# Performance work log

Hardware: AMD Instinct MI355X
Metric: run time of the kernel (lower is better)

## Reference

```python
import jax, jax.numpy as jnp
import numpy as np

N, K, DIN, DOUT = 50000, 16, 128, 64  # nodes per graph, fixed in-degree, feature dims


def setup_inputs() -> dict:
    key = jax.random.key(0)
    ks = jax.random.split(key, 9)
    s1 = 1.0 / np.sqrt(DIN)
    s2 = 1.0 / np.sqrt(2 * DOUT)
    return {
        "x1": jax.random.normal(ks[0], (N, DIN), jnp.float32),
        "x2": jax.random.normal(ks[1], (N, DIN), jnp.float32),
        "nbr1": jax.random.randint(ks[2], (N, K), 0, N, dtype=jnp.int32),
        "nbr2": jax.random.randint(ks[3], (N, K), 0, N, dtype=jnp.int32),
        "W_e1": jax.random.uniform(ks[4], (DIN, DOUT), jnp.float32, -s1, s1),
        "W_s1": jax.random.uniform(ks[5], (DIN, DOUT), jnp.float32, -s1, s1),
        "W_e2": jax.random.uniform(ks[6], (2 * DOUT, DOUT), jnp.float32, -s2, s2),
        "W_s2": jax.random.uniform(ks[7], (2 * DOUT, DOUT), jnp.float32, -s2, s2),
        "w_att": jax.random.uniform(ks[8], (2 * DOUT,), jnp.float32, -s2, s2),
    }


def _layer(x, nbr, We, Ws, norm):
    # CGNNConv: per-edge-type linear on sources, self linear on dests,
    # norm-weighted scatter-add aggregation, sigmoid(cat(self, aggr)).
    xn = x @ We                                      # [N, DOUT] source transform
    xs = x @ Ws                                      # [N, DOUT] self transform
    aggr = jnp.sum(norm[..., None] * xn[nbr], axis=1)  # [N, DOUT] fixed-degree segment sum
    return jax.nn.sigmoid(jnp.concatenate([xs, aggr], axis=1)), aggr


def _self_attn(aggr, nbr, w):
    # exp(leaky_relu(cat(aggr[dst], aggr[src]) @ w)), normalized over each dst's in-edges
    si = aggr @ w[:DOUT]            # dest contribution, [N]
    sj = (aggr @ w[DOUT:])[nbr]     # src contribution,  [N, K]
    e = jnp.exp(jax.nn.leaky_relu(si[:, None] + sj, 0.01))
    return e / jnp.sum(e, axis=1, keepdims=True)


def _cross_attn(aggr1, nbr1, aggr2, nbr2):
    # pairwise exp(-||a1_k - a2_l||) over each paired node's neighbor sets,
    # normalized by the total sum; att1 = row marginals, att2 = col marginals.
    a1, a2 = aggr1[nbr1], aggr2[nbr2]                # [N, K, DOUT]
    d2 = (jnp.sum(a1 * a1, -1)[:, :, None] + jnp.sum(a2 * a2, -1)[:, None, :]
          - 2.0 * jnp.einsum('nkd,nld->nkl', a1, a2))
    sim = jnp.exp(-jnp.sqrt(jnp.maximum(d2, 1e-12)))  # [N, K, K]
    total = jnp.sum(sim, axis=(1, 2), keepdims=True)  # [N, 1, 1]
    att1 = jnp.sum(sim, axis=2) / total[:, :, 0]      # [N, K]
    att2 = jnp.sum(sim, axis=1) / total[:, 0, :]      # [N, K]
    return att1, att2


def reference(x1, x2, nbr1, nbr2, W_e1, W_s1, W_e2, W_s2, w_att):
    inv_deg = jnp.full((N, K), 1.0 / K, dtype=x1.dtype)  # degree(col)^-1 with fixed degree K
    # layers 0 .. num_layers-2 use degree norm (shared weights across both graphs)
    h1, aggr1 = _layer(x1, nbr1, W_e1, W_s1, inv_deg)
    h2, aggr2 = _layer(x2, nbr2, W_e1, W_s1, inv_deg)
    # attention stages on last aggregates
    sa1 = _self_attn(aggr1, nbr1, w_att)
    sa2 = _self_attn(aggr2, nbr2, w_att)
    ca1, ca2 = _cross_attn(aggr1, nbr1, aggr2, nbr2)
    # final layer uses norm = cross_attention * self_attention per edge
    o1, _ = _layer(h1, nbr1, W_e2, W_s2, ca1 * sa1)
    o2, _ = _layer(h2, nbr2, W_e2, W_s2, ca2 * sa2)
    return o1, o2
```

## Files before the change

### kernel.cpp

```cpp
#include <hip/hip_runtime.h>
#include <hip/hip_bf16.h>

#define N_NODES 50000
#define K_NBR   16
#define DIN     128
#define DOUT    64
#define NPB     64

typedef __hip_bfloat16 bf16;
typedef __attribute__((ext_vector_type(8))) short bf16x8;
typedef __attribute__((ext_vector_type(4))) float f32x4;

__device__ __forceinline__ float b2f(bf16 v) { return __bfloat162float(v); }
__device__ __forceinline__ float us2f(unsigned short u) {
    return __uint_as_float(((unsigned)u) << 16);
}
__device__ __forceinline__ float sigmoidf_(float x) { return 1.0f / (1.0f + __expf(-x)); }
__device__ __forceinline__ short f2bs(float f) {
    bf16 b = __float2bfloat16(f);
    return *reinterpret_cast<short*>(&b);
}
__device__ __forceinline__ float readlane_f(float v, int lane) {
    return __uint_as_float(__builtin_amdgcn_readlane(__float_as_uint(v), lane));
}

template <typename T> __device__ __forceinline__ float ld(const T* p, size_t i);
template <> __device__ __forceinline__ float ld<float>(const float* p, size_t i) { return p[i]; }
template <> __device__ __forceinline__ float ld<bf16>(const bf16* p, size_t i)   { return b2f(p[i]); }

template <typename T> __device__ __forceinline__ void st(T* p, size_t i, float v);
template <> __device__ __forceinline__ void st<float>(float* p, size_t i, float v) { p[i] = v; }
template <> __device__ __forceinline__ void st<bf16>(bf16* p, size_t i, float v)   { p[i] = __float2bfloat16(v); }

__device__ __forceinline__ bf16x8 load_a8(const bf16* p) { return *(const bf16x8*)p; }
__device__ __forceinline__ bf16x8 load_a8(const float* p) {
    float4 v0 = *(const float4*)p;
    float4 v1 = *(const float4*)(p + 4);
    bf16x8 r;
    r[0] = f2bs(v0.x); r[1] = f2bs(v0.y); r[2] = f2bs(v0.z); r[3] = f2bs(v0.w);
    r[4] = f2bs(v1.x); r[5] = f2bs(v1.y); r[6] = f2bs(v1.z); r[7] = f2bs(v1.w);
    return r;
}

__global__ __launch_bounds__(256) void wtrans_kernel(
    const void* __restrict__ Wa, const void* __restrict__ Wb,
    const void* __restrict__ Wc, const void* __restrict__ Wd,
    const unsigned short* __restrict__ x1probe,
    unsigned short* __restrict__ wtg, int* __restrict__ flag)
{
    __shared__ unsigned short t[DIN][DOUT + 1];
    __shared__ int cnt;
    if (threadIdx.x == 0) cnt = 0;
    __syncthreads();
    int c = 0;
#pragma unroll
    for (int i = 0; i < 16; ++i) {
        unsigned short w = x1probe[(size_t)(threadIdx.x * 16 + i) * 2];
        int e = (w >> 7) & 0xFF;
        c += (e >= 112 && e <= 142) ? 1 : 0;
    }
    atomicAdd(&cnt, c);
    __syncthreads();
    const int isf32 = (cnt >= 2048) ? 0 : 1;
    if (blockIdx.x == 0 && threadIdx.x == 0) *flag = isf32;

    const void* W = (blockIdx.x == 0 ? Wa : blockIdx.x == 1 ? Wb : blockIdx.x == 2 ? Wc : Wd);
    unsigned short* o = wtg + (size_t)blockIdx.x * DIN * DOUT;
    if (isf32) {
        const float* Wf = (const float*)W;
#pragma unroll 8
        for (int it = 0; it < 32; ++it) {
            int idx = threadIdx.x + 256 * it;
            t[idx >> 6][idx & 63] = (unsigned short)f2bs(Wf[idx]);
        }
    } else {
        const unsigned short* Wh = (const unsigned short*)W;
#pragma unroll 8
        for (int it = 0; it < 32; ++it) {
            int idx = threadIdx.x + 256 * it;
            t[idx >> 6][idx & 63] = Wh[idx];
        }
    }
    __syncthreads();
#pragma unroll 8
    for (int it = 0; it < 32; ++it) {
        int idx = threadIdx.x + 256 * it;
        int d = idx >> 7, k = idx & 127;
        o[idx] = t[k][d];
    }
}

template <typename TX, typename TO>
__device__ __forceinline__ void lin_mfma_body(
    const TX* __restrict__ x,
    const unsigned short* __restrict__ wt2,
    bf16* __restrict__ xnh, TO* __restrict__ o,
    unsigned short* __restrict__ wt)
{
    const int tid = threadIdx.x;
    const int nbase = blockIdx.x * NPB;

#pragma unroll
    for (int it = 0; it < 8; ++it) {
        int idx = tid + 256 * it;
        int mt = idx >> 10, rem = idx & 1023;
        int r = rem >> 4, c = rem & 15;
        int4 v = *(const int4*)(wt2 + mt * 8192 + r * DIN + c * 8);
        *(int4*)(wt + mt * 8192 + r * DIN + ((c ^ (r & 15)) << 3)) = v;
    }
    __syncthreads();

    const int w = tid >> 6, lane = tid & 63;
    const int m = lane & 15, g = lane >> 4;

    int arow = nbase + w * 16 + m;
    if (arow >= N_NODES) arow = N_NODES - 1;
    const TX* xrow = x + (size_t)arow * DIN;

    f32x4 acc[2][4] = {};
#pragma unroll
    for (int ks = 0; ks < 4; ++ks) {
        bf16x8 a = load_a8(xrow + ks * 32 + g * 8);
        int slot = ((ks * 4 + g) ^ m) << 3;
#pragma unroll
        for (int mt = 0; mt < 2; ++mt)
#pragma unroll
        for (int nc = 0; nc < 4; ++nc) {
            bf16x8 b = *(const bf16x8*)(wt + mt * 8192 + (nc * 16 + m) * DIN + slot);
            acc[mt][nc] = __builtin_amdgcn_mfma_f32_16x16x32_bf16(a, b, acc[mt][nc], 0, 0, 0);
        }
    }

#pragma unroll
    for (int nc = 0; nc < 4; ++nc) {
#pragma unroll
        for (int j = 0; j < 4; ++j) {
            int n = nbase + w * 16 + g * 4 + j;
            if (n < N_NODES) {
                int d = nc * 16 + m;
                xnh[(size_t)n * DOUT + d] = __float2bfloat16(acc[0][nc][j]);
                st(o, (size_t)n * DIN + d, sigmoidf_(acc[1][nc][j]));
            }
        }
    }
}

__global__ __launch_bounds__(256) void lin1_kernel(
    const void* __restrict__ x1, const void* __restrict__ x2,
    const unsigned short* __restrict__ wtg,
    bf16* __restrict__ xnh1, bf16* __restrict__ xnh2,
    bf16* __restrict__ h1, bf16* __restrict__ h2,
    const int* __restrict__ flag)
{
    __shared__ __align__(16) unsigned short wt[2 * DOUT * DIN];
    const int g = blockIdx.y;
    const void* x   = g ? x2 : x1;
    bf16*       xnh = g ? xnh2 : xnh1;
    bf16*       h   = g ? h2 : h1;
    if (*flag) lin_mfma_body<float, bf16>((const float*)x, wtg, xnh, h, wt);
    else       lin_mfma_body<bf16,  bf16>((const bf16*)x,  wtg, xnh, h, wt);
}

__global__ __launch_bounds__(256) void lin2_kernel(
    const bf16* __restrict__ h1, const bf16* __restrict__ h2,
    const unsigned short* __restrict__ wtg,
    bf16* __restrict__ heh1, bf16* __restrict__ heh2,
    void* __restrict__ out, const int* __restrict__ flag)
{
    __shared__ __align__(16) unsigned short wt[2 * DOUT * DIN];
    const int g = blockIdx.y;
    const bf16* h   = g ? h2 : h1;
    bf16*       heh = g ? heh2 : heh1;
    if (*flag) lin_mfma_body<bf16, float>(h, wtg + 2 * 8192, heh,
                                          (float*)out + (size_t)g * N_NODES * DIN, wt);
    else       lin_mfma_body<bf16, bf16>(h, wtg + 2 * 8192, heh,
                                         (bf16*)out + (size_t)g * N_NODES * DIN, wt);
}

template <typename T>
__device__ __forceinline__ void aggr1_body(
    const int* __restrict__ nbr, const bf16* __restrict__ xnh,
    bf16* __restrict__ agh, bf16* __restrict__ h, const T* __restrict__ watt,
    float* __restrict__ qq, float* __restrict__ slo, float* __restrict__ shi)
{
    const int warp = __builtin_amdgcn_readfirstlane(threadIdx.x >> 6);
    const int lane = threadIdx.x & 63;
    const int n = blockIdx.x * 4 + warp;
    const int* __restrict__ nrow = nbr + n * K_NBR;
    const unsigned short* __restrict__ xu = (const unsigned short*)xnh;

    unsigned short xv[K_NBR];
#pragma unroll
    for (int k = 0; k < K_NBR; ++k)
        xv[k] = xu[(size_t)nrow[k] * DOUT + lane];

    float acc = 0.f;
#pragma unroll
    for (int k = 0; k < K_NBR; ++k) acc += us2f(xv[k]);
    acc *= (1.0f / K_NBR);
    bf16 av16 = __float2bfloat16(acc);
    float av = b2f(av16);
    agh[(size_t)n * DOUT + lane] = av16;
    h[(size_t)n * DIN + DOUT + lane] = __float2bfloat16(sigmoidf_(acc));

    float wl = ld(watt, lane);
    float wh = ld(watt, DOUT + lane);
    float pq = av * av;
    float pl = acc * wl;
    float ph = acc * wh;
#pragma unroll
    for (int off = 1; off < 64; off <<= 1) {
        pq += __shfl_xor(pq, off, 64);
        pl += __shfl_xor(pl, off, 64);
        ph += __shfl_xor(ph, off, 64);
    }
    if (lane == 0) { qq[n] = pq; slo[n] = pl; shi[n] = ph; }
}

__global__ __launch_bounds__(256) void aggr1_kernel(
    const int* __restrict__ nbr1, const int* __restrict__ nbr2,
    const bf16* __restrict__ xnh1, const bf16* __restrict__ xnh2,
    bf16* __restrict__ agh1, bf16* __restrict__ agh2,
    bf16* __restrict__ h1, bf16* __restrict__ h2,
    const void* __restrict__ watt,
    float* __restrict__ qq1, float* __restrict__ qq2,
    float* __restrict__ slo1, float* __restrict__ slo2,
    float* __restrict__ shi1, float* __restrict__ shi2,
    const int* __restrict__ flag)
{
    const int g = blockIdx.y;
    const int*  nbr = g ? nbr2 : nbr1;
    const bf16* xnh = g ? xnh2 : xnh1;
    bf16*       agh = g ? agh2 : agh1;
    bf16*       h   = g ? h2 : h1;
    float* qq  = g ? qq2  : qq1;
    float* slo = g ? slo2 : slo1;
    float* shi = g ? shi2 : shi1;
    if (*flag) aggr1_body<float>(nbr, xnh, agh, h, (const float*)watt, qq, slo, shi);
    else       aggr1_body<bf16>(nbr, xnh, agh, h, (const bf16*)watt,  qq, slo, shi);
}

template <typename TO>
__device__ __forceinline__ void attn_fused_body(
    const int* __restrict__ nbr1, const int* __restrict__ nbr2,
    const unsigned short* __restrict__ agh1, const unsigned short* __restrict__ agh2,
    const float* __restrict__ qq1, const float* __restrict__ qq2,
    const float* __restrict__ slo1, const float* __restrict__ slo2,
    const float* __restrict__ shi1, const float* __restrict__ shi2,
    const bf16* __restrict__ heh1, const bf16* __restrict__ heh2,
    TO* __restrict__ out)
{
    const int warp = __builtin_amdgcn_readfirstlane(threadIdx.x >> 6);
    const int lane = threadIdx.x & 63;
    const int n = blockIdx.x * 4 + warp;
    const int m = lane & 15, g = lane >> 4;

    const int* __restrict__ nrow1 = nbr1 + n * K_NBR;
    const int* __restrict__ nrow2 = nbr2 + n * K_NBR;
    const unsigned short* __restrict__ hu1 = (const unsigned short*)heh1;
    const unsigned short* __restrict__ hu2 = (const unsigned short*)heh2;

    unsigned short hv1[K_NBR], hv2[K_NBR];
#pragma unroll
    for (int k = 0; k < K_NBR; ++k) {
        hv1[k] = hu1[(size_t)nrow1[k] * DOUT + lane];
        hv2[k] = hu2[(size_t)nrow2[k] * DOUT + lane];
    }

    int idxr = 0;
    if (lane < 32) idxr = ((lane < 16) ? nbr1 : nbr2)[n * K_NBR + m];

    const int i1 = __shfl(idxr, m, 64);
    const int i2 = __shfl(idxr, 16 + m, 64);

    const bf16x8* a1p = (const bf16x8*)(agh1 + (size_t)i1 * DOUT + g * 8);
    const bf16x8* a2p = (const bf16x8*)(agh2 + (size_t)i2 * DOUT + g * 8);
    bf16x8 aA = a1p[0], aB = a1p[4];
    bf16x8 bA = a2p[0], bB = a2p[4];

    int myidx = __shfl(idxr, lane & 31, 64);
    const float* pa = (lane < 16) ? qq1 : (lane < 32) ? qq2 : (lane < 48) ? shi1 : shi2;
    float aux = pa[(size_t)myidx];

    float si  = (lane < 16) ? slo1[n] : slo2[n];
    float sjv = __shfl(aux, 32 + (lane & 31), 64);
    float v = si + sjv;
    v = v > 0.f ? v : 0.01f * v;
    float ev = __expf(v);
    float esum = ev;
#pragma unroll
    for (int off = 1; off < 16; off <<= 1) esum += __shfl_xor(esum, off, 64);

    f32x4 acc = {};
    acc = __builtin_amdgcn_mfma_f32_16x16x32_bf16(aA, bA, acc, 0, 0, 0);
    acc = __builtin_amdgcn_mfma_f32_16x16x32_bf16(aB, bB, acc, 0, 0, 0);

    float q2c = __shfl(aux, 16 + m, 64);
    float s0, s1, s2, s3;
    {
        float q10 = __shfl(aux, g * 4 + 0, 64);
        float q11 = __shfl(aux, g * 4 + 1, 64);
        float q12 = __shfl(aux, g * 4 + 2, 64);
        float q13 = __shfl(aux, g * 4 + 3, 64);
        s0 = __expf(-sqrtf(fmaxf(q10 + q2c - 2.f * acc[0], 1e-12f)));
        s1 = __expf(-sqrtf(fmaxf(q11 + q2c - 2.f * acc[1], 1e-12f)));
        s2 = __expf(-sqrtf(fmaxf(q12 + q2c - 2.f * acc[2], 1e-12f)));
        s3 = __expf(-sqrtf(fmaxf(q13 + q2c - 2.f * acc[3], 1e-12f)));
    }

    float c = s0 + s1 + s2 + s3;
#pragma unroll
    for (int off = 1; off < 16; off <<= 1) {
        s0 += __shfl_xor(s0, off, 64);
        s1 += __shfl_xor(s1, off, 64);
        s2 += __shfl_xor(s2, off, 64);
        s3 += __shfl_xor(s3, off, 64);
    }
    float cs = c;
    cs += __shfl_xor(cs, 16, 64);
    cs += __shfl_xor(cs, 32, 64);
    float tot = cs;
#pragma unroll
    for (int off = 1; off < 16; off <<= 1) tot += __shfl_xor(tot, off, 64);
    float rt = 1.0f / tot;

    float r0 = __shfl(s0, (m >> 2) << 4, 64);
    float r1 = __shfl(s1, (m >> 2) << 4, 64);
    float r2 = __shfl(s2, (m >> 2) << 4, 64);
    float r3 = __shfl(s3, (m >> 2) << 4, 64);
    int mr = m & 3;
    float rsm = mr == 0 ? r0 : mr == 1 ? r1 : mr == 2 ? r2 : r3;

    float wv = (g == 0) ? (rsm * rt * ev / esum)
             : (g == 1) ? (cs  * rt * ev / esum) : 0.f;

    float acc1 = 0.f, acc2 = 0.f;
#pragma unroll
    for (int k = 0; k < K_NBR; ++k) {
        acc1 += readlane_f(wv, k)      * us2f(hv1[k]);
        acc2 += readlane_f(wv, 16 + k) * us2f(hv2[k]);
    }
    st(out, (size_t)n * DIN + DOUT + lane, sigmoidf_(acc1));
    st(out, ((size_t)N_NODES + n) * DIN + DOUT + lane, sigmoidf_(acc2));
}

__global__ __launch_bounds__(256) void attn_kernel(
    const int* __restrict__ nbr1, const int* __restrict__ nbr2,
    const unsigned short* __restrict__ agh1, const unsigned short* __restrict__ agh2,
    const float* __restrict__ qq1, const float* __restrict__ qq2,
    const float* __restrict__ slo1, const float* __restrict__ slo2,
    const float* __restrict__ shi1, const float* __restrict__ shi2,
    const bf16* __restrict__ heh1, const bf16* __restrict__ heh2,
    void* __restrict__ out, const int* __restrict__ flag)
{
    if (*flag) attn_fused_body<float>(nbr1, nbr2, agh1, agh2, qq1, qq2, slo1, slo2,
                                      shi1, shi2, heh1, heh2, (float*)out);
    else       attn_fused_body<bf16>(nbr1, nbr2, agh1, agh2, qq1, qq2, slo1, slo2,
                                     shi1, shi2, heh1, heh2, (bf16*)out);
}

extern "C" void kernel_launch(void* const* d_in, const int* in_sizes, int n_in,
                              void* d_out, int out_size, void* d_ws, size_t ws_size,
                              hipStream_t stream)
{
    const void* x1   = d_in[0];
    const void* x2   = d_in[1];
    const int*  nbr1 = (const int*)d_in[2];
    const int*  nbr2 = (const int*)d_in[3];
    const void* We1  = d_in[4];
    const void* Ws1  = d_in[5];
    const void* We2  = d_in[6];
    const void* Ws2  = d_in[7];
    const void* watt = d_in[8];

    char* ws = (char*)d_ws;
    const size_t SZH  = (size_t)N_NODES * DOUT * sizeof(bf16);
    const size_t HSZ  = (size_t)N_NODES * DIN * sizeof(bf16);
    const size_t NSZ  = (size_t)N_NODES * sizeof(float);
    bf16* xnh1 = (bf16*)(ws + 0 * SZH);
    bf16* xnh2 = (bf16*)(ws + 1 * SZH);
    bf16* agh1 = (bf16*)(ws + 2 * SZH);
    bf16* agh2 = (bf16*)(ws + 3 * SZH);
    bf16* h1   = (bf16*)(ws + 4 * SZH);
    bf16* h2   = (bf16*)(ws + 4 * SZH + HSZ);
    char* p    =         ws + 4 * SZH + 2 * HSZ;
    int*  flag = (int*)  (p);
    char* aux  =          p + 4096;
    float* qq1  = (float*)(aux + 0 * NSZ);
    float* qq2  = (float*)(aux + 1 * NSZ);
    float* slo1 = (float*)(aux + 2 * NSZ);
    float* slo2 = (float*)(aux + 3 * NSZ);
    float* shi1 = (float*)(aux + 4 * NSZ);
    float* shi2 = (float*)(aux + 5 * NSZ);
    unsigned short* wtg = (unsigned short*)(aux + 6 * NSZ);

    dim3 b(256);
    dim3 g4(N_NODES / 4, 2);
    dim3 gl((N_NODES + NPB - 1) / NPB, 2);
    dim3 ga(N_NODES / 4);

    wtrans_kernel<<<dim3(4), b, 0, stream>>>(We1, Ws1, We2, Ws2,
                                             (const unsigned short*)x1, wtg, flag);
    lin1_kernel <<<gl, b, 0, stream>>>(x1, x2, wtg, xnh1, xnh2, h1, h2, flag);
    aggr1_kernel<<<g4, b, 0, stream>>>(nbr1, nbr2, xnh1, xnh2, agh1, agh2, h1, h2,
                                       watt, qq1, qq2, slo1, slo2, shi1, shi2, flag);
    lin2_kernel <<<gl, b, 0, stream>>>(h1, h2, wtg, xnh1, xnh2, d_out, flag);
    attn_kernel <<<ga, b, 0, stream>>>(nbr1, nbr2, (const unsigned short*)agh1,
                                       (const unsigned short*)agh2, qq1, qq2,
                                       slo1, slo2, shi1, shi2, xnh1, xnh2,
                                       d_out, flag);
}
```

Measured before the change: 230.2 us.

## Fuse first-layer aggregation with second-layer MFMA linear into one kernel

Measured after the change: 251.3 us. +9.1%, slower.

```diff
diff --git a/kernel.cpp b/kernel.cpp
--- a/kernel.cpp
+++ b/kernel.cpp
@@ -94,7 +94,7 @@
 __device__ __forceinline__ void lin_mfma_body(
     const TX* __restrict__ x,
     const unsigned short* __restrict__ wt2,
-    bf16* __restrict__ xnh, TO* __restrict__ o,
+    bf16* __restrict__ xnh, TO* __restrict__ o, const int ostride,
     unsigned short* __restrict__ wt)
 {
     const int tid = threadIdx.x;
@@ -139,7 +139,7 @@
             if (n < N_NODES) {
                 int d = nc * 16 + m;
                 xnh[(size_t)n * DOUT + d] = __float2bfloat16(acc[0][nc][j]);
-                st(o, (size_t)n * DIN + d, sigmoidf_(acc[1][nc][j]));
+                st(o, (size_t)n * ostride + d, sigmoidf_(acc[1][nc][j]));
             }
         }
     }
@@ -149,95 +149,140 @@
     const void* __restrict__ x1, const void* __restrict__ x2,
     const unsigned short* __restrict__ wtg,
     bf16* __restrict__ xnh1, bf16* __restrict__ xnh2,
-    bf16* __restrict__ h1, bf16* __restrict__ h2,
+    bf16* __restrict__ hlo1, bf16* __restrict__ hlo2,
     const int* __restrict__ flag)
 {
     __shared__ __align__(16) unsigned short wt[2 * DOUT * DIN];
     const int g = blockIdx.y;
     const void* x   = g ? x2 : x1;
     bf16*       xnh = g ? xnh2 : xnh1;
-    bf16*       h   = g ? h2 : h1;
-    if (*flag) lin_mfma_body<float, bf16>((const float*)x, wtg, xnh, h, wt);
-    else       lin_mfma_body<bf16,  bf16>((const bf16*)x,  wtg, xnh, h, wt);
-}
-
-__global__ __launch_bounds__(256) void lin2_kernel(
-    const bf16* __restrict__ h1, const bf16* __restrict__ h2,
-    const unsigned short* __restrict__ wtg,
-    bf16* __restrict__ heh1, bf16* __restrict__ heh2,
-    void* __restrict__ out, const int* __restrict__ flag)
-{
-    __shared__ __align__(16) unsigned short wt[2 * DOUT * DIN];
-    const int g = blockIdx.y;
-    const bf16* h   = g ? h2 : h1;
-    bf16*       heh = g ? heh2 : heh1;
-    if (*flag) lin_mfma_body<bf16, float>(h, wtg + 2 * 8192, heh,
-                                          (float*)out + (size_t)g * N_NODES * DIN, wt);
-    else       lin_mfma_body<bf16, bf16>(h, wtg + 2 * 8192, heh,
-                                         (bf16*)out + (size_t)g * N_NODES * DIN, wt);
-}
-
-template <typename T>
-__device__ __forceinline__ void aggr1_body(
+    bf16*       hlo = g ? hlo2 : hlo1;
+    if (*flag) lin_mfma_body<float, bf16>((const float*)x, wtg, xnh, hlo, DOUT, wt);
+    else       lin_mfma_body<bf16,  bf16>((const bf16*)x,  wtg, xnh, hlo, DOUT, wt);
+}
+
+template <typename TW, typename TO>
+__device__ __forceinline__ void aggmm_body(
     const int* __restrict__ nbr, const bf16* __restrict__ xnh,
-    bf16* __restrict__ agh, bf16* __restrict__ h, const T* __restrict__ watt,
-    float* __restrict__ qq, float* __restrict__ slo, float* __restrict__ shi)
-{
-    const int warp = __builtin_amdgcn_readfirstlane(threadIdx.x >> 6);
-    const int lane = threadIdx.x & 63;
-    const int n = blockIdx.x * 4 + warp;
-    const int* __restrict__ nrow = nbr + n * K_NBR;
-    const unsigned short* __restrict__ xu = (const unsigned short*)xnh;
-
-    unsigned short xv[K_NBR];
-#pragma unroll
-    for (int k = 0; k < K_NBR; ++k)
-        xv[k] = xu[(size_t)nrow[k] * DOUT + lane];
-
-    float acc = 0.f;
-#pragma unroll
-    for (int k = 0; k < K_NBR; ++k) acc += us2f(xv[k]);
-    acc *= (1.0f / K_NBR);
-    bf16 av16 = __float2bfloat16(acc);
-    float av = b2f(av16);
-    agh[(size_t)n * DOUT + lane] = av16;
-    h[(size_t)n * DIN + DOUT + lane] = __float2bfloat16(sigmoidf_(acc));
+    const bf16* __restrict__ hlo, const unsigned short* __restrict__ wt2,
+    const TW* __restrict__ watt,
+    bf16* __restrict__ agh, float* __restrict__ qq, float* __restrict__ slo,
+    float* __restrict__ shi, bf16* __restrict__ heh, TO* __restrict__ out,
+    unsigned short* __restrict__ ht, unsigned short* __restrict__ wt)
+{
+    const int tid = threadIdx.x;
+    const int w = tid >> 6, lane = tid & 63;
+    const int nbase = blockIdx.x * NPB;
+
+#pragma unroll
+    for (int it = 0; it < 8; ++it) {
+        int idx = tid + 256 * it;
+        int mt = idx >> 10, rem = idx & 1023;
+        int r = rem >> 4, c = rem & 15;
+        int4 v = *(const int4*)(wt2 + mt * 8192 + r * DIN + c * 8);
+        *(int4*)(wt + mt * 8192 + r * DIN + ((c ^ (r & 15)) << 3)) = v;
+    }
 
     float wl = ld(watt, lane);
     float wh = ld(watt, DOUT + lane);
-    float pq = av * av;
-    float pl = acc * wl;
-    float ph = acc * wh;
-#pragma unroll
-    for (int off = 1; off < 64; off <<= 1) {
-        pq += __shfl_xor(pq, off, 64);
-        pl += __shfl_xor(pl, off, 64);
-        ph += __shfl_xor(ph, off, 64);
-    }
-    if (lane == 0) { qq[n] = pq; slo[n] = pl; shi[n] = ph; }
-}
-
-__global__ __launch_bounds__(256) void aggr1_kernel(
+    const unsigned short* __restrict__ xu = (const unsigned short*)xnh;
+    const unsigned short* __restrict__ hu = (const unsigned short*)hlo;
+
+#pragma unroll 4
+    for (int j = 0; j < 16; ++j) {
+        int n = nbase + w * 16 + j;
+        int ncl = n < N_NODES ? n : N_NODES - 1;
+        const int* __restrict__ nrow = nbr + ncl * K_NBR;
+        unsigned short xv[K_NBR];
+#pragma unroll
+        for (int k = 0; k < K_NBR; ++k)
+            xv[k] = xu[(size_t)nrow[k] * DOUT + lane];
+        unsigned short hl = hu[(size_t)ncl * DOUT + lane];
+
+        float acc = 0.f;
+#pragma unroll
+        for (int k = 0; k < K_NBR; ++k) acc += us2f(xv[k]);
+        acc *= (1.0f / K_NBR);
+        bf16 av16 = __float2bfloat16(acc);
+        float av = b2f(av16);
+
+        const int r = w * 16 + j;
+        ht[r * DIN + ((((lane >> 3) ^ j) << 3) | (lane & 7))] = hl;
+        ht[r * DIN + (((((lane >> 3) | 8) ^ j) << 3) | (lane & 7))] =
+            (unsigned short)f2bs(sigmoidf_(acc));
+
+        if (n < N_NODES) agh[(size_t)n * DOUT + lane] = av16;
+
+        float pq = av * av, pl = acc * wl, ph = acc * wh;
+#pragma unroll
+        for (int off = 1; off < 64; off <<= 1) {
+            pq += __shfl_xor(pq, off, 64);
+            pl += __shfl_xor(pl, off, 64);
+            ph += __shfl_xor(ph, off, 64);
+        }
+        if (lane == 0 && n < N_NODES) { qq[n] = pq; slo[n] = pl; shi[n] = ph; }
+    }
+    __syncthreads();
+
+    const int m = lane & 15, g = lane >> 4;
+    f32x4 acc2[2][4] = {};
+    const unsigned short* hrow = ht + (w * 16 + m) * DIN;
+#pragma unroll
+    for (int ks = 0; ks < 4; ++ks) {
+        int slot = ((ks * 4 + g) ^ m) << 3;
+        bf16x8 a = *(const bf16x8*)(hrow + slot);
+#pragma unroll
+        for (int mt = 0; mt < 2; ++mt)
+#pragma unroll
+        for (int nc = 0; nc < 4; ++nc) {
+            bf16x8 b = *(const bf16x8*)(wt + mt * 8192 + (nc * 16 + m) * DIN + slot);
+            acc2[mt][nc] = __builtin_amdgcn_mfma_f32_16x16x32_bf16(a, b, acc2[mt][nc], 0, 0, 0);
+        }
+    }
+#pragma unroll
+    for (int nc = 0; nc < 4; ++nc) {
+#pragma unroll
+        for (int j2 = 0; j2 < 4; ++j2) {
+            int n = nbase + w * 16 + g * 4 + j2;
+            if (n < N_NODES) {
+                int d = nc * 16 + m;
+                heh[(size_t)n * DOUT + d] = __float2bfloat16(acc2[0][nc][j2]);
+                st(out, (size_t)n * DIN + d, sigmoidf_(acc2[1][nc][j2]));
+            }
+        }
+    }
+}
+
+__global__ __launch_bounds__(256) void aggmm_kernel(
     const int* __restrict__ nbr1, const int* __restrict__ nbr2,
     const bf16* __restrict__ xnh1, const bf16* __restrict__ xnh2,
+    const bf16* __restrict__ hlo1, const bf16* __restrict__ hlo2,
+    const unsigned short* __restrict__ wtg, const void* __restrict__ watt,
     bf16* __restrict__ agh1, bf16* __restrict__ agh2,
-    bf16* __restrict__ h1, bf16* __restrict__ h2,
-    const void* __restrict__ watt,
     float* __restrict__ qq1, float* __restrict__ qq2,
     float* __restrict__ slo1, float* __restrict__ slo2,
     float* __restrict__ shi1, float* __restrict__ shi2,
-    const int* __restrict__ flag)
-{
+    bf16* __restrict__ heh1, bf16* __restrict__ heh2,
+    void* __restrict__ out, const int* __restrict__ flag)
+{
+    __shared__ __align__(16) unsigned short ht[NPB * DIN];
+    __shared__ __align__(16) unsigned short wt[2 * DOUT * DIN];
     const int g = blockIdx.y;
     const int*  nbr = g ? nbr2 : nbr1;
     const bf16* xnh = g ? xnh2 : xnh1;
-    bf16*       agh = g ? agh2 : agh1;
-    bf16*       h   = g ? h2 : h1;
+    const bf16* hlo = g ? hlo2 : hlo1;
+    bf16*  agh = g ? agh2 : agh1;
     float* qq  = g ? qq2  : qq1;
     float* slo = g ? slo2 : slo1;
     float* shi = g ? shi2 : shi1;
-    if (*flag) aggr1_body<float>(nbr, xnh, agh, h, (const float*)watt, qq, slo, shi);
-    else       aggr1_body<bf16>(nbr, xnh, agh, h, (const bf16*)watt,  qq, slo, shi);
+    bf16*  heh = g ? heh2 : heh1;
+    const unsigned short* wt2 = wtg + 2 * 8192;
+    if (*flag)
+        aggmm_body<float, float>(nbr, xnh, hlo, wt2, (const float*)watt, agh, qq, slo,
+                                 shi, heh, (float*)out + (size_t)g * N_NODES * DIN, ht, wt);
+    else
+        aggmm_body<bf16, bf16>(nbr, xnh, hlo, wt2, (const bf16*)watt, agh, qq, slo,
+                               shi, heh, (bf16*)out + (size_t)g * N_NODES * DIN, ht, wt);
 }
 
 template <typename TO>
@@ -374,16 +419,17 @@
     const void* watt = d_in[8];
 
     char* ws = (char*)d_ws;
-    const size_t SZH  = (size_t)N_NODES * DOUT * sizeof(bf16);
-    const size_t HSZ  = (size_t)N_NODES * DIN * sizeof(bf16);
-    const size_t NSZ  = (size_t)N_NODES * sizeof(float);
+    const size_t SZH = (size_t)N_NODES * DOUT * sizeof(bf16);
+    const size_t NSZ = (size_t)N_NODES * sizeof(float);
     bf16* xnh1 = (bf16*)(ws + 0 * SZH);
     bf16* xnh2 = (bf16*)(ws + 1 * SZH);
     bf16* agh1 = (bf16*)(ws + 2 * SZH);
     bf16* agh2 = (bf16*)(ws + 3 * SZH);
-    bf16* h1   = (bf16*)(ws + 4 * SZH);
-    bf16* h2   = (bf16*)(ws + 4 * SZH + HSZ);
-    char* p    =         ws + 4 * SZH + 2 * HSZ;
+    bf16* hlo1 = (bf16*)(ws + 4 * SZH);
+    bf16* hlo2 = (bf16*)(ws + 5 * SZH);
+    bf16* heh1 = (bf16*)(ws + 6 * SZH);
+    bf16* heh2 = (bf16*)(ws + 7 * SZH);
+    char* p    =         ws + 8 * SZH;
     int*  flag = (int*)  (p);
     char* aux  =          p + 4096;
     float* qq1  = (float*)(aux + 0 * NSZ);
@@ -395,18 +441,17 @@
     unsigned short* wtg = (unsigned short*)(aux + 6 * NSZ);
 
     dim3 b(256);
-    dim3 g4(N_NODES / 4, 2);
     dim3 gl((N_NODES + NPB - 1) / NPB, 2);
     dim3 ga(N_NODES / 4);
 
     wtrans_kernel<<<dim3(4), b, 0, stream>>>(We1, Ws1, We2, Ws2,
                                              (const unsigned short*)x1, wtg, flag);
-    lin1_kernel <<<gl, b, 0, stream>>>(x1, x2, wtg, xnh1, xnh2, h1, h2, flag);
-    aggr1_kernel<<<g4, b, 0, stream>>>(nbr1, nbr2, xnh1, xnh2, agh1, agh2, h1, h2,
-                                       watt, qq1, qq2, slo1, slo2, shi1, shi2, flag);
-    lin2_kernel <<<gl, b, 0, stream>>>(h1, h2, wtg, xnh1, xnh2, d_out, flag);
+    lin1_kernel <<<gl, b, 0, stream>>>(x1, x2, wtg, xnh1, xnh2, hlo1, hlo2, flag);
+    aggmm_kernel<<<gl, b, 0, stream>>>(nbr1, nbr2, xnh1, xnh2, hlo1, hlo2, wtg, watt,
+                                       agh1, agh2, qq1, qq2, slo1, slo2, shi1, shi2,
+                                       heh1, heh2, d_out, flag);
     attn_kernel <<<ga, b, 0, stream>>>(nbr1, nbr2, (const unsigned short*)agh1,
                                        (const unsigned short*)agh2, qq1, qq2,
-                                       slo1, slo2, shi1, shi2, xnh1, xnh2,
+                                       slo1, slo2, shi1, shi2, heh1, heh2,
                                        d_out, flag);
 }
```
